# Kernel optimization log

Hardware: AMD Instinct MI355X
Metric: run time of the kernel (lower is better)

## Reference

```python
import jax, jax.numpy as jnp
import numpy as np
from jax import lax

DN = ('NCHW', 'OIHW', 'NCHW')

def conv(x, w, b):
    y = lax.conv_general_dilated(x, w, (1, 1), 'VALID', dimension_numbers=DN)
    return y + b[None, :, None, None]

def maxpool2(x):
    return lax.reduce_window(x, -jnp.inf, lax.max, (1, 1, 2, 2), (1, 1, 2, 2), 'VALID')

def setup_inputs() -> dict:
    key = jax.random.key(0)
    ks = jax.random.split(key, 16)
    s = 0.05
    return {
        'x': jax.random.normal(ks[0], (8192, 1, 28, 28), jnp.float32),
        'kf_w1': jax.random.normal(ks[1], (8, 1, 7, 7), jnp.float32) * s,
        'kf_b1': jax.random.normal(ks[2], (8,), jnp.float32) * s,
        'kf_w2': jax.random.normal(ks[3], (10, 8, 5, 5), jnp.float32) * s,
        'kf_b2': jax.random.normal(ks[4], (10,), jnp.float32) * s,
        'kf_fc1_w': jax.random.normal(ks[5], (32, 90), jnp.float32) * s,
        'kf_fc1_b': jax.random.normal(ks[6], (32,), jnp.float32) * s,
        'kf_fc2_w': jax.random.normal(ks[7], (40, 32), jnp.float32) * s,
        'kf_fc2_b': jax.random.normal(ks[8], (40,), jnp.float32) * s,
        'conv2_w': jax.random.normal(ks[9], (20, 10, 5, 5), jnp.float32) * s,
        'conv2_b': jax.random.normal(ks[10], (20,), jnp.float32) * s,
        'fc1_w': jax.random.normal(ks[11], (50, 320), jnp.float32) * s,
        'fc1_b': jax.random.normal(ks[12], (50,), jnp.float32) * s,
        'fc2_w': jax.random.normal(ks[13], (10, 50), jnp.float32) * s,
        'fc2_b': jax.random.normal(ks[14], (10,), jnp.float32) * s,
    }

def _forward(x, kf_w1, kf_b1, kf_w2, kf_b2, kf_fc1_w, kf_fc1_b, kf_fc2_w, kf_fc2_b,
             conv2_w, conv2_b, fc1_w, fc1_b, fc2_w, fc2_b):
    n = x.shape[0]
    # KernelFinder: conv7 -> pool -> relu -> conv5 -> pool -> relu
    f = jax.nn.relu(maxpool2(conv(x, kf_w1, kf_b1)))        # [N,8,11,11]
    f = jax.nn.relu(maxpool2(conv(f, kf_w2, kf_b2)))        # [N,10,3,3]
    f = f.reshape(n, 90)
    h = jax.nn.relu(f @ kf_fc1_w.T + kf_fc1_b)
    kernels = (h @ kf_fc2_w.T + kf_fc2_b).reshape(n, 10, 1, 2, 2)
    # per-sample dynamic conv: each image gets its own [10,1,2,2] kernel
    def one(img, k):
        return lax.conv_general_dilated(img[None], k, (1, 1), 'VALID',
                                        dimension_numbers=DN)[0]
    y = jax.vmap(one)(x, kernels)                           # [N,10,27,27]
    y = jax.nn.relu(maxpool2(y))                            # [N,10,13,13]
    # dropout2d is identity in eval mode
    y = jax.nn.relu(maxpool2(conv(y, conv2_w, conv2_b)))    # [N,20,4,4]
    y = y.reshape(n, 320)
    y = jax.nn.relu(y @ fc1_w.T + fc1_b)
    # F.dropout identity in eval
    y = y @ fc2_w.T + fc2_b
    return jax.nn.log_softmax(y, axis=1)

def reference(x, kf_w1, kf_b1, kf_w2, kf_b2, kf_fc1_w, kf_fc1_b, kf_fc2_w, kf_fc2_b,
              conv2_w, conv2_b, fc1_w, fc1_b, fc2_w, fc2_b):
    return _forward(x, kf_w1, kf_b1, kf_w2, kf_b2, kf_fc1_w, kf_fc1_b, kf_fc2_w,
                    kf_fc2_b, conv2_w, conv2_b, fc1_w, fc1_b, fc2_w, fc2_b)
```

## Files before the change

kernel.cpp:

```cpp
#include <hip/hip_runtime.h>
#include <math.h>

#define TPB 192

typedef __attribute__((ext_vector_type(8))) short bf16x8;
typedef __attribute__((ext_vector_type(4))) float f32x4;

#define OX    0
#define OC1B  784
#define OC5   1312
#define OY2   784
#define OF    2656
#define OH    2748
#define OC2S  2656
#define OK2   4960
#define OP3   0
#define OPF   320
#define OA1   420
#define OZ    472
#define SM_TOT 5000

#define W3U 0
#define W5U 9600
#define WSU_TOT 13184

__device__ __forceinline__ unsigned short f2bf(float f) {
    unsigned int u = __float_as_uint(f);
    u += 0x7FFF + ((u >> 16) & 1);
    return (unsigned short)(u >> 16);
}

__global__ void repack_w(const float* __restrict__ conv2_w,
                         const float* __restrict__ kf_w2,
                         unsigned short* __restrict__ ws)
{
    int i = blockIdx.x * blockDim.x + threadIdx.x;
    if (i < 9600) {
        int g = i / 640, rem = i % 640;
        int oc = rem >> 5, k = rem & 31;
        int kyp = g % 3, kx = g / 3;
        int kyip = k >> 4, ic = k & 15, ky = 2 * kyp + kyip;
        float v = 0.f;
        if (ic < 10 && ky < 5)
            v = conv2_w[(oc * 10 + ic) * 25 + ky * 5 + kx];
        ws[W3U + i] = f2bf(v);
    } else if (i < WSU_TOT) {
        int j = i - 9600;
        int s = j >> 9, rem = j & 511;
        int oc = rem >> 5, k = rem & 31;
        int tap = 4 * s + (k >> 3), ic = k & 7;
        float v = 0.f;
        if (oc < 10 && tap < 25)
            v = kf_w2[(oc * 8 + ic) * 25 + tap];
        ws[W5U + j] = f2bf(v);
    }
}

__global__ __launch_bounds__(TPB) void fused_forward(
    const float* __restrict__ x,
    const float* __restrict__ kf_w1, const float* __restrict__ kf_b1,
    const float* __restrict__ kf_w2, const float* __restrict__ kf_b2,
    const float* __restrict__ kf_fc1_w, const float* __restrict__ kf_fc1_b,
    const float* __restrict__ kf_fc2_w, const float* __restrict__ kf_fc2_b,
    const float* __restrict__ conv2_w, const float* __restrict__ conv2_b,
    const float* __restrict__ fc1_w, const float* __restrict__ fc1_b,
    const float* __restrict__ fc2_w, const float* __restrict__ fc2_b,
    const unsigned short* __restrict__ wsu,
    float* __restrict__ out)
{
    __shared__ __align__(16) float sm[SM_TOT];
    const int tid = threadIdx.x;
    const int n = blockIdx.x;

    {
        const float4* xg = (const float4*)(x + (long long)n * 784);
        float4* d = (float4*)&sm[OX];
        for (int i = tid; i < 196; i += TPB) d[i] = xg[i];
    }
    __syncthreads();

    if (tid < 176) {
        int oc = tid & 7;
        int r  = tid >> 3;
        int py = r >> 1;
        int h  = r & 1;
        const int cc0 = 10 * h;
        float c[2][12];
        #pragma unroll
        for (int r2 = 0; r2 < 2; ++r2)
            #pragma unroll
            for (int i = 0; i < 12; ++i) c[r2][i] = 0.f;
        float wc[7], wp[7];
        const float* wg = kf_w1 + oc * 49;
        #pragma unroll
        for (int i = 0; i < 7; ++i) wc[i] = wg[i];
        #pragma unroll
        for (int t = 0; t < 8; ++t) {
            const float2* xs = (const float2*)&sm[OX + (2 * py + t) * 28 + cc0];
            float row[18];
            #pragma unroll
            for (int i = 0; i < 9; ++i) { float2 q = xs[i]; row[2*i] = q.x; row[2*i+1] = q.y; }
            if (t <= 6) {
                #pragma unroll
                for (int kx = 0; kx < 7; ++kx)
                    #pragma unroll
                    for (int cc = 0; cc < 12; ++cc)
                        c[0][cc] = fmaf(wc[kx], row[cc + kx], c[0][cc]);
            }
            if (t >= 1) {
                #pragma unroll
                for (int kx = 0; kx < 7; ++kx)
                    #pragma unroll
                    for (int cc = 0; cc < 12; ++cc)
                        c[1][cc] = fmaf(wp[kx], row[cc + kx], c[1][cc]);
            }
            #pragma unroll
            for (int i = 0; i < 7; ++i) wp[i] = wc[i];
            if (t < 7) {
                const float* wn = wg + (t + 1) * 7;
                #pragma unroll
                for (int i = 0; i < 7; ++i) wc[i] = wn[i];
            }
        }
        float b = kf_b1[oc];
        unsigned short* c1b = (unsigned short*)&sm[OC1B];
        #pragma unroll
        for (int j = 0; j < 6; ++j) {
            float m = fmaxf(fmaxf(c[0][2 * j], c[0][2 * j + 1]),
                            fmaxf(c[1][2 * j], c[1][2 * j + 1]));
            c1b[py * 96 + (5 * h + j) * 8 + oc] = f2bf(fmaxf(m + b, 0.f));
        }
    }
    __syncthreads();

    {
        const int wv = tid >> 6, l = tid & 63;
        const int lm = l & 15, lq = l >> 4;
        int nn = wv * 16 + lm;
        int nc = nn > 35 ? 35 : nn;
        const int rr = nc / 6, cc = nc - rr * 6;
        const unsigned short* c1b = (const unsigned short*)&sm[OC1B];
        const char* W5 = (const char*)(wsu + W5U);
        f32x4 acc = {0.f, 0.f, 0.f, 0.f};
        #pragma unroll
        for (int s = 0; s < 7; ++s) {
            int tap = 4 * s + lq;
            int ky = (tap * 13) >> 6;
            int kx = tap - ky * 5;
            bf16x8 A = *(const bf16x8*)(W5 + s * 1024 + lm * 64 + lq * 16);
            bf16x8 B = *(const bf16x8*)(c1b + (rr + ky) * 96 + (cc + kx) * 8);
            acc = __builtin_amdgcn_mfma_f32_16x16x32_bf16(A, B, acc, 0, 0, 0);
        }
        *(f32x4*)(&sm[OC5] + nn * 20 + lq * 4) = acc;
    }
    __syncthreads();

    if (tid < 90) {
        int oc = tid % 10, rr = tid / 10;
        int py = rr / 3, px = rr % 3;
        const float* C5 = &sm[OC5];
        int nb = (2 * py) * 6 + 2 * px;
        float v = fmaxf(fmaxf(C5[nb * 20 + oc], C5[(nb + 1) * 20 + oc]),
                        fmaxf(C5[(nb + 6) * 20 + oc], C5[(nb + 7) * 20 + oc]));
        sm[OF + oc * 9 + rr] = fmaxf(v + kf_b2[oc], 0.f);
    }
    __syncthreads();

    if (tid < 32) {
        float acc = kf_fc1_b[tid];
        const float2* wr = (const float2*)&kf_fc1_w[tid * 90];
        const float2* ff = (const float2*)&sm[OF];
        for (int i = 0; i < 45; ++i) {
            float2 wv = wr[i], fv = ff[i];
            acc = fmaf(wv.x, fv.x, acc);
            acc = fmaf(wv.y, fv.y, acc);
        }
        sm[OH + tid] = fmaxf(acc, 0.f);
    }
    if (tid < 40) {
        float acc = kf_fc2_b[tid];
        const float4* wr = (const float4*)&kf_fc2_w[tid * 32];
        const float4* hh = (const float4*)&sm[OH];
        #pragma unroll
        for (int i = 0; i < 8; ++i) {
            float4 wv = wr[i], hv = hh[i];
            acc = fmaf(wv.x, hv.x, acc);
            acc = fmaf(wv.y, hv.y, acc);
            acc = fmaf(wv.z, hv.z, acc);
            acc = fmaf(wv.w, hv.w, acc);
        }
        sm[OK2 + tid] = acc;
    }
    if (tid >= 64) {
        float4* z4 = (float4*)&sm[OY2];
        for (int i = tid - 64; i < 468; i += 128) z4[i] = float4{0.f, 0.f, 0.f, 0.f};
    }
    __syncthreads();

    if (tid < 120) {
        int oc = tid % 10, py = tid / 10;
        float4 kv = *(const float4*)&sm[OK2 + oc * 4];
        float k0 = kv.x, k1 = kv.y, k2 = kv.z, k3 = kv.w;
        const float* x0 = &sm[OX + 2 * py * 28];
        const float* x1 = x0 + 28;
        const float* x2 = x0 + 56;
        float2 q0 = *(const float2*)&x0[0];
        float2 q1 = *(const float2*)&x1[0];
        float2 q2 = *(const float2*)&x2[0];
        float A0 = q0.x, B0 = q0.y;
        float A1 = q1.x, B1 = q1.y;
        float A2 = q2.x, B2 = q2.y;
        unsigned short* y2 = (unsigned short*)&sm[OY2];
        #pragma unroll
        for (int j = 0; j < 12; ++j) {
            float2 r0 = *(const float2*)&x0[2 * j + 2];
            float2 r1 = *(const float2*)&x1[2 * j + 2];
            float2 r2v = *(const float2*)&x2[2 * j + 2];
            float C0 = r0.x, C1 = r1.x, C2 = r2v.x;
            float c00 = A0 * k0 + B0 * k1 + A1 * k2 + B1 * k3;
            float c01 = B0 * k0 + C0 * k1 + B1 * k2 + C1 * k3;
            float c10 = A1 * k0 + B1 * k1 + A2 * k2 + B2 * k3;
            float c11 = B1 * k0 + C1 * k1 + B2 * k2 + C2 * k3;
            float m = fmaxf(fmaxf(c00, c01), fmaxf(c10, c11));
            y2[py * 288 + j * 24 + oc] = f2bf(fmaxf(m, 0.f));
            A0 = C0; A1 = C1; A2 = C2;
            B0 = r0.y; B1 = r1.y; B2 = r2v.y;
        }
    }
    __syncthreads();

    {
        const int wv = tid >> 6;
        if (wv < 2) {
            const int l  = tid & 63;
            const int lm = l & 15, lk = l >> 4;
            f32x4 a00 = {0.f, 0.f, 0.f, 0.f};
            f32x4 a01 = a00, a10 = a00, a11 = a00;
            const char* W3 = (const char*)(wsu + W3U);
            const int aoff0 = lm * 64 + lk * 16;
            const int oc1 = 16 + (lm < 4 ? lm : 3);
            const int aoff1 = oc1 * 64 + lk * 16;
            const int n0 = wv * 32 + lm;
            const int n1 = n0 + 16;
            const int kyip = l >> 5, icb = (lk & 1) * 8;
            const unsigned short* Y2 = (const unsigned short*)&sm[OY2];
            const int b0 = ((n0 >> 3) + kyip) * 288 + (n0 & 7) * 24 + icb;
            const int b1 = ((n1 >> 3) + kyip) * 288 + (n1 & 7) * 24 + icb;
            #pragma unroll
            for (int p = 0; p < 3; ++p) {
                #pragma unroll
                for (int kx = 0; kx < 5; ++kx) {
                    const char* wa = W3 + (kx * 3 + p) * 1280;
                    bf16x8 A0 = *(const bf16x8*)(wa + aoff0);
                    bf16x8 A1 = *(const bf16x8*)(wa + aoff1);
                    const int bo = p * 576 + kx * 24;
                    bf16x8 B0 = *(const bf16x8*)(Y2 + b0 + bo);
                    bf16x8 B1 = *(const bf16x8*)(Y2 + b1 + bo);
                    a00 = __builtin_amdgcn_mfma_f32_16x16x32_bf16(A0, B0, a00, 0, 0, 0);
                    a01 = __builtin_amdgcn_mfma_f32_16x16x32_bf16(A0, B1, a01, 0, 0, 0);
                    a10 = __builtin_amdgcn_mfma_f32_16x16x32_bf16(A1, B0, a10, 0, 0, 0);
                    a11 = __builtin_amdgcn_mfma_f32_16x16x32_bf16(A1, B1, a11, 0, 0, 0);
                }
            }
            float* C = &sm[OC2S];
            *(f32x4*)(C + n0 * 36 + lk * 4)      = a00;
            *(f32x4*)(C + n1 * 36 + lk * 4)      = a01;
            *(f32x4*)(C + n0 * 36 + 16 + lk * 4) = a10;
            *(f32x4*)(C + n1 * 36 + 16 + lk * 4) = a11;
        }
    }
    __syncthreads();

    if (tid < 80) {
        int oc = tid % 20, py = tid / 20;
        float b = conv2_b[oc];
        const float* C = &sm[OC2S];
        #pragma unroll
        for (int px = 0; px < 4; ++px) {
            int n00 = (2 * py) * 8 + 2 * px;
            float c00 = C[n00 * 36 + oc];
            float c01 = C[(n00 + 1) * 36 + oc];
            float c10 = C[(n00 + 8) * 36 + oc];
            float c11 = C[(n00 + 9) * 36 + oc];
            float m = fmaxf(fmaxf(c00, c01), fmaxf(c10, c11)) + b;
            sm[OP3 + oc * 16 + py * 4 + px] = fmaxf(m, 0.f);
        }
    }
    __syncthreads();

    if (tid < 100) {
        int g = tid / 50, o = tid % 50;
        const float4* wr4 = (const float4*)&fc1_w[o * 320 + g * 160];
        const float4* pp4 = (const float4*)&sm[OP3 + g * 160];
        float acc = 0.f;
        for (int i = 0; i < 40; ++i) {
            float4 wv = wr4[i], pv = pp4[i];
            acc = fmaf(wv.x, pv.x, acc);
            acc = fmaf(wv.y, pv.y, acc);
            acc = fmaf(wv.z, pv.z, acc);
            acc = fmaf(wv.w, pv.w, acc);
        }
        sm[OPF + tid] = acc;
    }
    __syncthreads();

    if (tid < 50) {
        float acc = fc1_b[tid] + sm[OPF + tid] + sm[OPF + 50 + tid];
        sm[OA1 + tid] = fmaxf(acc, 0.f);
    }
    if (tid < 10) {
        float acc = fc2_b[tid];
        const float2* wr = (const float2*)&fc2_w[tid * 50];
        #pragma unroll
        for (int i = 0; i < 25; ++i) {
            float2 wv = wr[i];
            acc = fmaf(wv.x, sm[OA1 + 2 * i], acc);
            acc = fmaf(wv.y, sm[OA1 + 2 * i + 1], acc);
        }
        sm[OZ + tid] = acc;
    }
    if (tid < 10) {
        float m = sm[OZ + 0];
        #pragma unroll
        for (int i = 1; i < 10; ++i) m = fmaxf(m, sm[OZ + i]);
        float s = 0.f;
        #pragma unroll
        for (int i = 0; i < 10; ++i) s += expf(sm[OZ + i] - m);
        out[n * 10 + tid] = sm[OZ + tid] - m - logf(s);
    }
}

extern "C" void kernel_launch(void* const* d_in, const int* in_sizes, int n_in,
                              void* d_out, int out_size, void* d_ws, size_t ws_size,
                              hipStream_t stream) {
    const float* x        = (const float*)d_in[0];
    const float* kf_w1    = (const float*)d_in[1];
    const float* kf_b1    = (const float*)d_in[2];
    const float* kf_w2    = (const float*)d_in[3];
    const float* kf_b2    = (const float*)d_in[4];
    const float* kf_fc1_w = (const float*)d_in[5];
    const float* kf_fc1_b = (const float*)d_in[6];
    const float* kf_fc2_w = (const float*)d_in[7];
    const float* kf_fc2_b = (const float*)d_in[8];
    const float* conv2_w  = (const float*)d_in[9];
    const float* conv2_b  = (const float*)d_in[10];
    const float* fc1_w    = (const float*)d_in[11];
    const float* fc1_b    = (const float*)d_in[12];
    const float* fc2_w    = (const float*)d_in[13];
    const float* fc2_b    = (const float*)d_in[14];

    const int N = in_sizes[0] / 784;

    unsigned short* wsu = (unsigned short*)d_ws;
    repack_w<<<(WSU_TOT + 255) / 256, 256, 0, stream>>>(conv2_w, kf_w2, wsu);

    fused_forward<<<N, TPB, 0, stream>>>(
        x, kf_w1, kf_b1, kf_w2, kf_b2, kf_fc1_w, kf_fc1_b, kf_fc2_w, kf_fc2_b,
        conv2_w, conv2_b, fc1_w, fc1_b, fc2_w, fc2_b, wsu, (float*)d_out);
}
```

Measured before the change: 230.5 us.

## Compute first 7x7 conv with bf16 MFMA via staged im2col in LDS

```diff
diff --git a/kernel.cpp b/kernel.cpp
--- a/kernel.cpp
+++ b/kernel.cpp
@@ -7,22 +7,27 @@
 typedef __attribute__((ext_vector_type(4))) float f32x4;
 
 #define OX    0
-#define OC1B  784
-#define OC5   1312
+#define OXB0  784
+#define OXB1  1264
+#define OXI   1744
+#define OC7   4816
+#define OC1B  6736
+#define OC5   1744
 #define OY2   784
-#define OF    2656
-#define OH    2748
-#define OC2S  2656
-#define OK2   4960
+#define OF    2704
+#define OH    2796
+#define OK2   2828
+#define OC2S  2868
 #define OP3   0
 #define OPF   320
 #define OA1   420
 #define OZ    472
-#define SM_TOT 5000
+#define SM_TOT 7264
 
 #define W3U 0
 #define W5U 9600
-#define WSU_TOT 13184
+#define W7U 13184
+#define WSU_TOT 14208
 
 __device__ __forceinline__ unsigned short f2bf(float f) {
     unsigned int u = __float_as_uint(f);
@@ -32,6 +37,7 @@
 
 __global__ void repack_w(const float* __restrict__ conv2_w,
                          const float* __restrict__ kf_w2,
+                         const float* __restrict__ kf_w1,
                          unsigned short* __restrict__ ws)
 {
     int i = blockIdx.x * blockDim.x + threadIdx.x;
@@ -44,7 +50,7 @@
         if (ic < 10 && ky < 5)
             v = conv2_w[(oc * 10 + ic) * 25 + ky * 5 + kx];
         ws[W3U + i] = f2bf(v);
-    } else if (i < WSU_TOT) {
+    } else if (i < 13184) {
         int j = i - 9600;
         int s = j >> 9, rem = j & 511;
         int oc = rem >> 5, k = rem & 31;
@@ -53,6 +59,14 @@
         if (oc < 10 && tap < 25)
             v = kf_w2[(oc * 8 + ic) * 25 + tap];
         ws[W5U + j] = f2bf(v);
+    } else if (i < WSU_TOT) {
+        int j = i - 13184;
+        int s = j >> 9, oc = (j >> 5) & 15, k = j & 31;
+        int ky = s * 4 + (k >> 3), kx = k & 7;
+        float v = 0.f;
+        if (oc < 8 && kx < 7 && ky < 7)
+            v = kf_w1[oc * 49 + ky * 7 + kx];
+        ws[W7U + j] = f2bf(v);
     }
 }
 
@@ -72,66 +86,99 @@
     const int tid = threadIdx.x;
     const int n = blockIdx.x;
 
+    const float bias1 = kf_b1[tid & 7];
+
     {
         const float4* xg = (const float4*)(x + (long long)n * 784);
         float4* d = (float4*)&sm[OX];
         for (int i = tid; i < 196; i += TPB) d[i] = xg[i];
-    }
-    __syncthreads();
-
-    if (tid < 176) {
-        int oc = tid & 7;
-        int r  = tid >> 3;
-        int py = r >> 1;
-        int h  = r & 1;
-        const int cc0 = 10 * h;
-        float c[2][12];
-        #pragma unroll
-        for (int r2 = 0; r2 < 2; ++r2)
+        float4* z4 = (float4*)&sm[OXB0];
+        for (int i = tid; i < 240; i += TPB) z4[i] = float4{0.f, 0.f, 0.f, 0.f};
+    }
+    __syncthreads();
+
+    if (tid < 196) {
+        float4 v = *(const float4*)&sm[OX + tid * 4];
+        unsigned short* b0 = (unsigned short*)&sm[OXB0];
+        unsigned short* b1 = (unsigned short*)&sm[OXB1];
+        #pragma unroll
+        for (int j = 0; j < 4; ++j) {
+            int e = tid * 4 + j;
+            int row = e / 28, c = e - row * 28;
+            unsigned short bv = f2bf(((const float*)&v)[j]);
+            int pos = row * 32 + c;
+            b0[pos] = bv;
+            if (pos > 0) b1[pos - 1] = bv;
+        }
+    }
+    __syncthreads();
+
+    auto stageXi = [&](int it) {
+        unsigned short* Xi = (unsigned short*)&sm[OXI];
+        const int* b0 = (const int*)&sm[OXB0];
+        const int* b1 = (const int*)&sm[OXB1];
+        #pragma unroll
+        for (int i = 0; i < 4; ++i) {
+            int t = tid + 192 * i;
+            int nn = t % 96, ky = t / 96;
+            int pp = nn >= 48 ? 1 : 0;
+            int rem = nn - pp * 48;
+            int rr = rem >= 24 ? 1 : 0;
+            int col = rem - rr * 24;
+            int row = 4 * it + 2 * pp + rr + ky;
+            row = row > 29 ? 29 : row;
+            const int* src = (col & 1) ? (b1 + row * 16 + (col >> 1))
+                                       : (b0 + row * 16 + (col >> 1));
+            int4 w4;
+            w4.x = src[0]; w4.y = src[1]; w4.z = src[2]; w4.w = src[3];
+            *(int4*)(Xi + nn * 64 + ((ky * 8) ^ ((nn & 7) << 3))) = w4;
+        }
+    };
+
+    stageXi(0);
+    __syncthreads();
+
+    for (int it = 0; it < 6; ++it) {
+        {
+            const int wv = tid >> 6, l = tid & 63;
+            const int lm = l & 15, lk = l >> 4;
+            const unsigned short* Xi = (const unsigned short*)&sm[OXI];
+            const unsigned short* W7 = wsu + W7U;
+            const int n0 = wv * 16 + lm, n1 = n0 + 48;
+            f32x4 acc0 = {0.f, 0.f, 0.f, 0.f};
+            f32x4 acc1 = {0.f, 0.f, 0.f, 0.f};
             #pragma unroll
-            for (int i = 0; i < 12; ++i) c[r2][i] = 0.f;
-        float wc[7], wp[7];
-        const float* wg = kf_w1 + oc * 49;
-        #pragma unroll
-        for (int i = 0; i < 7; ++i) wc[i] = wg[i];
-        #pragma unroll
-        for (int t = 0; t < 8; ++t) {
-            const float2* xs = (const float2*)&sm[OX + (2 * py + t) * 28 + cc0];
-            float row[18];
-            #pragma unroll
-            for (int i = 0; i < 9; ++i) { float2 q = xs[i]; row[2*i] = q.x; row[2*i+1] = q.y; }
-            if (t <= 6) {
-                #pragma unroll
-                for (int kx = 0; kx < 7; ++kx)
-                    #pragma unroll
-                    for (int cc = 0; cc < 12; ++cc)
-                        c[0][cc] = fmaf(wc[kx], row[cc + kx], c[0][cc]);
+            for (int s = 0; s < 2; ++s) {
+                bf16x8 A = *(const bf16x8*)(W7 + s * 512 + lm * 32 + lk * 8);
+                bf16x8 B0 = *(const bf16x8*)(Xi + n0 * 64 + ((s * 32 + lk * 8) ^ ((n0 & 7) << 3)));
+                bf16x8 B1 = *(const bf16x8*)(Xi + n1 * 64 + ((s * 32 + lk * 8) ^ ((n1 & 7) << 3)));
+                acc0 = __builtin_amdgcn_mfma_f32_16x16x32_bf16(A, B0, acc0, 0, 0, 0);
+                acc1 = __builtin_amdgcn_mfma_f32_16x16x32_bf16(A, B1, acc1, 0, 0, 0);
             }
-            if (t >= 1) {
-                #pragma unroll
-                for (int kx = 0; kx < 7; ++kx)
-                    #pragma unroll
-                    for (int cc = 0; cc < 12; ++cc)
-                        c[1][cc] = fmaf(wp[kx], row[cc + kx], c[1][cc]);
+            float* C7 = &sm[OC7];
+            *(f32x4*)(C7 + n0 * 20 + lk * 4) = acc0;
+            *(f32x4*)(C7 + n1 * 20 + lk * 4) = acc1;
+        }
+        __syncthreads();
+
+        if (it < 5) stageXi(it + 1);
+        if (tid < 176) {
+            int oc = tid & 7, r = tid >> 3;
+            int c = r % 11, pp = r / 11;
+            int p = 2 * it + pp;
+            if (p < 11) {
+                const float* C7 = &sm[OC7];
+                int nb = pp * 48 + 2 * c;
+                float v00 = C7[nb * 20 + oc];
+                float v01 = C7[(nb + 1) * 20 + oc];
+                float v10 = C7[(nb + 24) * 20 + oc];
+                float v11 = C7[(nb + 25) * 20 + oc];
+                float m = fmaxf(fmaxf(v00, v01), fmaxf(v10, v11)) + bias1;
+                ((unsigned short*)&sm[OC1B])[p * 96 + c * 8 + oc] = f2bf(fmaxf(m, 0.f));
             }
-            #pragma unroll
-            for (int i = 0; i < 7; ++i) wp[i] = wc[i];
-            if (t < 7) {
-                const float* wn = wg + (t + 1) * 7;
-                #pragma unroll
-                for (int i = 0; i < 7; ++i) wc[i] = wn[i];
-            }
-        }
-        float b = kf_b1[oc];
-        unsigned short* c1b = (unsigned short*)&sm[OC1B];
-        #pragma unroll
-        for (int j = 0; j < 6; ++j) {
-            float m = fmaxf(fmaxf(c[0][2 * j], c[0][2 * j + 1]),
-                            fmaxf(c[1][2 * j], c[1][2 * j + 1]));
-            c1b[py * 96 + (5 * h + j) * 8 + oc] = f2bf(fmaxf(m + b, 0.f));
-        }
-    }
-    __syncthreads();
+        }
+        __syncthreads();
+    }
 
     {
         const int wv = tid >> 6, l = tid & 63;
@@ -352,7 +399,7 @@
     const int N = in_sizes[0] / 784;
 
     unsigned short* wsu = (unsigned short*)d_ws;
-    repack_w<<<(WSU_TOT + 255) / 256, 256, 0, stream>>>(conv2_w, kf_w2, wsu);
+    repack_w<<<(WSU_TOT + 255) / 256, 256, 0, stream>>>(conv2_w, kf_w2, kf_w1, wsu);
 
     fused_forward<<<N, TPB, 0, stream>>>(
         x, kf_w1, kf_b1, kf_w2, kf_b2, kf_fc1_w, kf_fc1_b, kf_fc2_w, kf_fc2_b,
```

After: 247.5 us. 1.07x slower.
